# Kernel optimization log

Hardware: AMD Instinct MI355X
Metric: run time of the kernel (lower is better)

The kernel has to match this reference:

```python
import jax, jax.numpy as jnp
import numpy as np
import math

B, C, L = 64, 16, 4096
EMB, DEPTH, NEXP = 256, 2, 4
SHAPE, STRIDE = 8, 4
NPATCH = (L - SHAPE) // STRIDE + 1  # 1023
SPARSE = 0.5
NF = 32

def gelu(x):
    return jax.nn.gelu(x, approximate=False)

def conv1d(x, w, stride=1, pad=0):
    return jax.lax.conv_general_dilated(x, w, (stride,), [(pad, pad)],
                                        dimension_numbers=('NCH', 'OIH', 'NCH'))

def rmsnorm(x, g):
    # F.normalize(x, dim=-1) * gamma * sqrt(D)
    n = jnp.sqrt(jnp.sum(x * x, axis=-1, keepdims=True))
    return x / jnp.maximum(n, 1e-12) * g * (x.shape[-1] ** 0.5)

def setup_inputs():
    ks = jax.random.split(jax.random.key(0), 16)
    r = lambda i, s: jax.random.normal(ks[i], s, jnp.float32) * 0.02
    return dict(
        x=jax.random.normal(ks[0], (B, C, L), jnp.float32),
        epoch=100, warm_up=50,
        emb_w=r(1, (EMB, C, SHAPE)), emb_b=jnp.zeros((EMB,), jnp.float32),
        pos_embed=r(2, (1, NPATCH, EMB)),
        attn_w1=r(3, (EMB, 8)), attn_b1=jnp.zeros((8,), jnp.float32),
        attn_w2=r(4, (8, 1)), attn_b2=jnp.zeros((1,), jnp.float32),
        gate_w=r(5, (EMB, NEXP)), gate_b=jnp.zeros((NEXP,), jnp.float32),
        ex_w1=r(6, (NEXP, EMB, EMB)), ex_b1=jnp.zeros((NEXP, EMB), jnp.float32),
        ex_w2=r(7, (NEXP, EMB, EMB)), ex_b2=jnp.zeros((NEXP, EMB), jnp.float32),
        moe_gamma=jnp.ones((EMB,), jnp.float32),
        norm1_g=jnp.ones((DEPTH, EMB), jnp.float32),
        norm2_g=jnp.ones((DEPTH, EMB), jnp.float32),
        bott_w=r(8, (DEPTH, NF, EMB, 1)),
        conv_w39=r(9, (DEPTH, NF, NF, 39)),
        conv_w19=r(10, (DEPTH, NF, NF, 19)),
        conv_w9=r(11, (DEPTH, NF, NF, 9)),
        mp_w=r(12, (DEPTH, NF, EMB, 1)),
        bn_g=jnp.ones((DEPTH, 4 * NF), jnp.float32),
        bn_b=jnp.zeros((DEPTH, 4 * NF), jnp.float32),
        proj_w=r(13, (DEPTH, 4 * NF, EMB)),
        proj_b=jnp.zeros((DEPTH, EMB), jnp.float32),
        head_w=r(14, (EMB, 1)), head_b=jnp.zeros((1,), jnp.float32),
    )

def _forward(x, epoch, warm_up, emb_w, emb_b, pos_embed, attn_w1, attn_b1,
             attn_w2, attn_b2, gate_w, gate_b, ex_w1, ex_b1, ex_w2, ex_b2,
             moe_gamma, norm1_g, norm2_g, bott_w, conv_w39, conv_w19, conv_w9,
             mp_w, bn_g, bn_b, proj_w, proj_b, head_w, head_b):
    def attn(h):  # (B,N,D) -> (B,N,1) sigmoid importance scores
        return jax.nn.sigmoid(jnp.tanh(h @ attn_w1 + attn_b1) @ attn_w2 + attn_b2)

    def moe(h):  # top-1 routed MoE; compute all experts densely, select via one-hot
        Bm, Nm, D = h.shape
        hf = h.reshape(-1, D)  # (T, D)
        logits = jax.nn.softmax(hf @ gate_w + gate_b, axis=-1)  # (T, E)
        top_idx = jnp.argmax(logits, axis=-1)
        top_val = jnp.max(logits, axis=-1, keepdims=True)
        mid = gelu(jnp.einsum('td,edh->eth', hf, ex_w1) + ex_b1[:, None, :])
        ye = jnp.einsum('eth,ehd->etd', mid, ex_w2) + ex_b2[:, None, :]
        sel = jax.nn.one_hot(top_idx, NEXP, dtype=h.dtype)  # (T, E)
        out = jnp.einsum('etd,te->td', ye, sel)
        y = rmsnorm((hf + out * top_val).reshape(Bm, Nm, D), moe_gamma)
        imp = logits.sum(0)
        load = jnp.var(imp, ddof=1) / (imp.mean() ** 2 + 1e-10)
        return gelu(y), load

    def inception(xc, i):  # xc: (B, D, T) -> (B, 4*NF, T)
        xb = conv1d(xc, bott_w[i])  # bottleneck 1x1 -> NF channels
        mp = jax.lax.reduce_window(xc, -jnp.inf, jax.lax.max, (1, 1, 3),
                                   (1, 1, 1), [(0, 0), (0, 0), (1, 1)])
        out = jnp.concatenate([conv1d(xb, conv_w39[i], pad=19),
                               conv1d(xb, conv_w19[i], pad=9),
                               conv1d(xb, conv_w9[i], pad=4),
                               conv1d(mp, mp_w[i])], axis=1)
        # BatchNorm1d eval mode: running mean 0 / var 1, affine gamma/beta
        out = out * (bn_g[i] / np.float32(np.sqrt(1.0 + 1e-5)))[None, :, None] \
              + bn_b[i][None, :, None]
        return gelu(out)

    def incep_branch(h, i):  # (B,N,D) -> (B,N,D)
        io = inception(jnp.transpose(h, (0, 2, 1)), i)
        return jnp.transpose(io, (0, 2, 1)) @ proj_w[i] + proj_b[i]

    h = conv1d(x, emb_w, stride=STRIDE) + emb_b[None, :, None]  # (B, EMB, N)
    h = jnp.transpose(h, (0, 2, 1)) + pos_embed  # N == NPATCH -> no interp
    # pos_drop is identity at inference

    schedule = np.linspace(0.0, SPARSE, DEPTH)
    total_loss = jnp.zeros((), h.dtype)
    end_scores = None
    for i in range(DEPTH):
        ratio = 1.0 if epoch < warm_up else 1.0 - float(schedule[i])
        is_last = (i == DEPTH - 1)
        N = h.shape[1]
        x_n = rmsnorm(h, norm1_g[i])
        scores = attn(x_n)  # (B, N, 1)
        if ratio < 1.0 and N > 2:
            left_k = max(math.ceil(ratio * N), 1)
            xs = x_n * scores
            idx = jnp.sort(jax.lax.top_k(scores[..., 0], left_k)[1], axis=1)
            left_x = jnp.take_along_axis(xs, idx[:, :, None], axis=1)
            # sum of non-topk tokens == total sum minus topk sum
            extra = xs.sum(1, keepdims=True) - left_x.sum(1, keepdims=True)
            h = jnp.concatenate([left_x, extra], axis=1)  # (B, left_k+1, D)
            x_n2 = rmsnorm(h, norm2_g[i])
            moe_out, loss = moe(x_n2)
            h = h + moe_out + incep_branch(x_n2, i)
            total_loss = total_loss + loss
        else:
            h = x_n * scores
            h = h + incep_branch(rmsnorm(h, norm2_g[i]), i)
        if is_last:
            end_scores = attn(h)  # dropout identity; scores on pre-gelu x
        h = gelu(h)
    logits = h @ head_w + head_b  # (B, N', 1)
    cls = (logits * end_scores).mean(axis=1)  # (B, 1)
    return cls[..., 0], total_loss

def reference(x, epoch, warm_up, emb_w, emb_b, pos_embed, attn_w1, attn_b1,
              attn_w2, attn_b2, gate_w, gate_b, ex_w1, ex_b1, ex_w2, ex_b2,
              moe_gamma, norm1_g, norm2_g, bott_w, conv_w39, conv_w19, conv_w9,
              mp_w, bn_g, bn_b, proj_w, proj_b, head_w, head_b):
    return _forward(x, epoch, warm_up, emb_w, emb_b, pos_embed, attn_w1,
                    attn_b1, attn_w2, attn_b2, gate_w, gate_b, ex_w1, ex_b1,
                    ex_w2, ex_b2, moe_gamma, norm1_g, norm2_g, bott_w,
                    conv_w39, conv_w19, conv_w9, mp_w, bn_g, bn_b, proj_w,
                    proj_b, head_w, head_b)
```

## Files before the change

kernel.cpp:

```cpp
#include <hip/hip_runtime.h>
#include <math.h>

#define BB 64
#define EMB 256
#define N0 1023
#define N1 513
#define NTOK0 (BB * N0)
#define NTOK1 (BB * N1)
#define GCH 16

typedef __attribute__((ext_vector_type(8))) short short8;
typedef __attribute__((ext_vector_type(4))) float f32x4;

__device__ __forceinline__ float gelu_f(float x) {
    return 0.5f * x * (1.0f + erff(x * 0.7071067811865476f));
}

__device__ __forceinline__ float4 gelu4(float4 v) {
    return make_float4(gelu_f(v.x), gelu_f(v.y), gelu_f(v.z), gelu_f(v.w));
}

__device__ __forceinline__ float wave_reduce(float v) {
#pragma unroll
    for (int o = 32; o > 0; o >>= 1) v += __shfl_down(v, o, 64);
    return v;
}

__device__ __forceinline__ unsigned short f2bf(float f) {
    unsigned int u = __float_as_uint(f);
    u = (u + 0x7FFFu + ((u >> 16) & 1u)) >> 16;
    return (unsigned short)u;
}
__device__ __forceinline__ float bf2f(unsigned short h) {
    return __uint_as_float(((unsigned int)h) << 16);
}

__global__ void convert_bf16(const float* __restrict__ ew1, const float* __restrict__ ew2,
                             const float* __restrict__ pjw,
                             const float* __restrict__ cw39, const float* __restrict__ cw19,
                             const float* __restrict__ cw9, const float* __restrict__ embw,
                             const float* __restrict__ bott, const float* __restrict__ mpw,
                             unsigned short* __restrict__ w1t, unsigned short* __restrict__ w2t,
                             unsigned short* __restrict__ pjwb,
                             unsigned short* __restrict__ cwh, unsigned short* __restrict__ cwl,
                             unsigned short* __restrict__ ewh, unsigned short* __restrict__ ewl,
                             unsigned short* __restrict__ bth, unsigned short* __restrict__ btl,
                             unsigned short* __restrict__ mph, unsigned short* __restrict__ mpl,
                             float* __restrict__ imp, int* __restrict__ counts) {
    int idx = blockIdx.x * 256 + threadIdx.x;
    if (blockIdx.x == 0 && threadIdx.x >= 252) {
        int i = threadIdx.x - 252;
        imp[i] = 0.0f; counts[i] = 0;
    }
    if (idx < 262144) {
        int e = idx >> 16, r = idx & 65535, n = r >> 8, k = r & 255;
        w1t[idx] = f2bf(ew1[(e << 16) + (k << 8) + n]);
    } else if (idx < 524288) {
        int j = idx - 262144;
        int e = j >> 16, r = j & 65535, n = r >> 8, k = r & 255;
        w2t[j] = f2bf(ew2[(e << 16) + (k << 8) + n]);
    } else if (idx < 589824) {
        int j = idx - 524288;
        int d = j >> 15, r = j & 32767, n = r >> 7, k = r & 127;
        pjwb[j] = f2bf(pjw[(d << 15) + (k << 8) + n]);
    } else if (idx < 727040) {
        int j = idx - 589824;
        int d = j / 68608, r = j % 68608;
        const float* src; int KT, rr;
        if (r < 39936)      { src = cw39; KT = 39; rr = r; }
        else if (r < 59392) { src = cw19; KT = 19; rr = r - 39936; }
        else                { src = cw9;  KT = 9;  rr = r - 59392; }
        int KK = KT * 32;
        int fo = rr / KK, jj = rr % KK, k = jj >> 5, fi = jj & 31;
        float w = src[(((d * 32 + fo) * 32) + fi) * KT + k];
        unsigned short h = f2bf(w);
        cwh[j] = h;
        cwl[j] = f2bf(w - bf2f(h));
    } else if (idx < 759808) {
        int j = idx - 727040;
        float w = embw[j];
        unsigned short h = f2bf(w);
        ewh[j] = h;
        ewl[j] = f2bf(w - bf2f(h));
    } else if (idx < 776192) {
        int j = idx - 759808;
        float w = bott[j];
        unsigned short h = f2bf(w);
        bth[j] = h;
        btl[j] = f2bf(w - bf2f(h));
    } else if (idx < 792576) {
        int j = idx - 776192;
        float w = mpw[j];
        unsigned short h = f2bf(w);
        mph[j] = h;
        mpl[j] = f2bf(w - bf2f(h));
    }
}

__global__ __launch_bounds__(256, 2)
void embed_mfma(const float* __restrict__ x, const unsigned short* __restrict__ ewh,
                const unsigned short* __restrict__ ewl, const float* __restrict__ emb_b,
                const float* __restrict__ pos, float* __restrict__ A) {
    int b = blockIdx.y;
    int n0 = blockIdx.x * 64;
    __shared__ __align__(16) unsigned short tokh[64 * 128];
    __shared__ __align__(16) unsigned short tokl[64 * 128];
    int tid = threadIdx.x;
#pragma unroll
    for (int it = 0; it < 4; it++) {
        int idx = tid + it * 256;
        int m = idx & 63, c = idx >> 6;
        int tok = n0 + m;
        float v[8] = {0.f, 0.f, 0.f, 0.f, 0.f, 0.f, 0.f, 0.f};
        if (tok < N0) {
            const float* p = x + ((size_t)b * 16 + c) * 4096 + 4 * tok;
            float4 a = *(const float4*)p;
            float4 bq = *(const float4*)(p + 4);
            v[0] = a.x; v[1] = a.y; v[2] = a.z; v[3] = a.w;
            v[4] = bq.x; v[5] = bq.y; v[6] = bq.z; v[7] = bq.w;
        }
        short8 hv, lv;
#pragma unroll
        for (int j = 0; j < 8; j++) {
            unsigned short hh = f2bf(v[j]);
            hv[j] = (short)hh;
            lv[j] = (short)f2bf(v[j] - bf2f(hh));
        }
        int si = (m << 7) + ((c << 3) ^ ((m & 7) << 3));
        *(short8*)(&tokh[si]) = hv;
        *(short8*)(&tokl[si]) = lv;
    }
    __syncthreads();

    int lane = tid & 63, wid = tid >> 6;
    int nb = wid << 6;
    int arow = lane & 15;
    int kgrp = (lane >> 4) << 3;
    int rb = (lane >> 4) << 2;

    f32x4 acc[4][4];
#pragma unroll
    for (int mt = 0; mt < 4; mt++)
#pragma unroll
        for (int nt = 0; nt < 4; nt++) acc[mt][nt] = f32x4{0.f, 0.f, 0.f, 0.f};

    for (int ks = 0; ks < 4; ks++) {
        int kk = (ks << 5) + kgrp;
        short8 ah[4], al[4], bh[4], bl[4];
#pragma unroll
        for (int mt = 0; mt < 4; mt++) {
            int m = (mt << 4) + arow;
            int si = (m << 7) + (kk ^ ((m & 7) << 3));
            ah[mt] = *(const short8*)(&tokh[si]);
            al[mt] = *(const short8*)(&tokl[si]);
        }
#pragma unroll
        for (int nt = 0; nt < 4; nt++) {
            int n = nb + (nt << 4) + arow;
            bh[nt] = *(const short8*)(&ewh[(n << 7) + kk]);
            bl[nt] = *(const short8*)(&ewl[(n << 7) + kk]);
        }
#pragma unroll
        for (int mt = 0; mt < 4; mt++) {
#pragma unroll
            for (int nt = 0; nt < 4; nt++) {
                acc[mt][nt] = __builtin_amdgcn_mfma_f32_16x16x32_bf16(ah[mt], bh[nt], acc[mt][nt], 0, 0, 0);
                acc[mt][nt] = __builtin_amdgcn_mfma_f32_16x16x32_bf16(al[mt], bh[nt], acc[mt][nt], 0, 0, 0);
                acc[mt][nt] = __builtin_amdgcn_mfma_f32_16x16x32_bf16(ah[mt], bl[nt], acc[mt][nt], 0, 0, 0);
            }
        }
    }

    float eb[4];
#pragma unroll
    for (int nt = 0; nt < 4; nt++) eb[nt] = emb_b[nb + (nt << 4) + arow];
#pragma unroll
    for (int mt = 0; mt < 4; mt++) {
#pragma unroll
        for (int nt = 0; nt < 4; nt++) {
            int n = nb + (nt << 4) + arow;
#pragma unroll
            for (int r = 0; r < 4; r++) {
                int m = (mt << 4) + rb + r;
                int tok = n0 + m;
                if (tok < N0)
                    A[((size_t)b * N0 + tok) * 256 + n] =
                        acc[mt][nt][r] + eb[nt] + pos[(size_t)tok * 256 + n];
            }
        }
    }
}

__global__ void norm_attn_kernel(const float* __restrict__ in, float* __restrict__ outv,
                                 float* __restrict__ score_out, const float* __restrict__ g,
                                 const float* __restrict__ w1, const float* __restrict__ b1,
                                 const float* __restrict__ w2, const float* __restrict__ b2,
                                 int scale_out, int pregelu,
                                 float* __restrict__ outv2, const float* __restrict__ g2,
                                 int T) {
    int wid = threadIdx.x >> 6, lane = threadIdx.x & 63;
    int t = blockIdx.x * 4 + wid;
    if (t >= T) return;
    float4 v = ((const float4*)(in + (size_t)t * 256))[lane];
    if (pregelu) v = gelu4(v);
    float4 xn = v;
    if (g != nullptr) {
        float ss = v.x * v.x + v.y * v.y + v.z * v.z + v.w * v.w;
        ss = wave_reduce(ss);
        ss = __shfl(ss, 0, 64);
        float inv = 16.0f / fmaxf(sqrtf(ss), 1e-12f);
        float4 g4 = ((const float4*)g)[lane];
        xn.x = v.x * inv * g4.x; xn.y = v.y * inv * g4.y;
        xn.z = v.z * inv * g4.z; xn.w = v.w * inv * g4.w;
    }
    float p[8];
#pragma unroll
    for (int j = 0; j < 8; j++) p[j] = 0.0f;
    const float xv[4] = {xn.x, xn.y, xn.z, xn.w};
#pragma unroll
    for (int c = 0; c < 4; c++) {
        const float4* wr = (const float4*)(w1 + (4 * lane + c) * 8);
        float4 wa = wr[0], wb = wr[1];
        float xx = xv[c];
        p[0] += xx * wa.x; p[1] += xx * wa.y; p[2] += xx * wa.z; p[3] += xx * wa.w;
        p[4] += xx * wb.x; p[5] += xx * wb.y; p[6] += xx * wb.z; p[7] += xx * wb.w;
    }
#pragma unroll
    for (int j = 0; j < 8; j++) p[j] = wave_reduce(p[j]);
    float sc = 0.0f;
    if (lane == 0) {
        float z = b2[0];
#pragma unroll
        for (int j = 0; j < 8; j++) z += tanhf(p[j] + b1[j]) * w2[j];
        sc = 1.0f / (1.0f + expf(-z));
        if (score_out) score_out[t] = sc;
    }
    sc = __shfl(sc, 0, 64);
    if (outv) {
        float m = scale_out ? sc : 1.0f;
        float4 o = make_float4(xn.x * m, xn.y * m, xn.z * m, xn.w * m);
        ((float4*)(outv + (size_t)t * 256))[lane] = o;
    }
    if (outv2) {
        float ss2 = xn.x * xn.x + xn.y * xn.y + xn.z * xn.z + xn.w * xn.w;
        ss2 = wave_reduce(ss2);
        ss2 = __shfl(ss2, 0, 64);
        float inv2 = 16.0f / fmaxf(sqrtf(ss2), 1e-12f);
        float4 q4 = ((const float4*)g2)[lane];
        float4 o;
        o.x = xn.x * inv2 * q4.x; o.y = xn.y * inv2 * q4.y;
        o.z = xn.z * inv2 * q4.z; o.w = xn.w * inv2 * q4.w;
        ((float4*)(outv2 + (size_t)t * 256))[lane] = o;
    }
}

__global__ void rmsnorm_kernel(const float* __restrict__ in, float* __restrict__ out,
                               const float* __restrict__ g, int T) {
    int wid = threadIdx.x >> 6, lane = threadIdx.x & 63;
    int t = blockIdx.x * 4 + wid;
    if (t >= T) return;
    float4 v = ((const float4*)(in + (size_t)t * 256))[lane];
    float ss = v.x * v.x + v.y * v.y + v.z * v.z + v.w * v.w;
    ss = wave_reduce(ss);
    ss = __shfl(ss, 0, 64);
    float inv = 16.0f / fmaxf(sqrtf(ss), 1e-12f);
    float4 g4 = ((const float4*)g)[lane];
    float4 o;
    o.x = v.x * inv * g4.x; o.y = v.y * inv * g4.y;
    o.z = v.z * inv * g4.z; o.w = v.w * inv * g4.w;
    ((float4*)(out + (size_t)t * 256))[lane] = o;
}

__global__ __launch_bounds__(256, 2)
void pw_mfma(const float* __restrict__ xn, const unsigned short* __restrict__ bwh,
             const unsigned short* __restrict__ bwl, const unsigned short* __restrict__ mwh,
             const unsigned short* __restrict__ mwl, const float* __restrict__ bng,
             const float* __restrict__ bnb, float* __restrict__ xb,
             float* __restrict__ cat, int N) {
    int b = blockIdx.y;
    int t0 = blockIdx.x * 32;
    __shared__ __align__(16) unsigned short xth[34 * 256];
    __shared__ __align__(16) unsigned short xtl[34 * 256];
    __shared__ __align__(16) unsigned short xmh[32 * 256];
    __shared__ __align__(16) unsigned short xml[32 * 256];
    const float* xbase = xn + (size_t)b * N * 256;
    int tid = threadIdx.x;
    for (int idx = tid; idx < 34 * 32; idx += 256) {
        int r = idx >> 5, p = (idx & 31) << 3;
        int t = t0 - 1 + r;
        short8 hv, lv;
        if (t >= 0 && t < N) {
            const float4* q = (const float4*)(xbase + (size_t)t * 256 + p);
            float4 a = q[0], c = q[1];
            float v[8] = {a.x, a.y, a.z, a.w, c.x, c.y, c.z, c.w};
#pragma unroll
            for (int j = 0; j < 8; j++) {
                unsigned short hh = f2bf(v[j]);
                hv[j] = (short)hh;
                lv[j] = (short)f2bf(v[j] - bf2f(hh));
            }
        } else {
#pragma unroll
            for (int j = 0; j < 8; j++) { hv[j] = (short)0xFF80; lv[j] = 0; }
        }
        int si = (r << 8) + (p ^ ((r & 7) << 3));
        *(short8*)(&xth[si]) = hv;
        *(short8*)(&xtl[si]) = lv;
    }
    __syncthreads();
    for (int idx = tid; idx < 32 * 32; idx += 256) {
        int r = idx >> 5, p = (idx & 31) << 3;
        int s0 = ((r + 0) << 8) + (p ^ (((r + 0) & 7) << 3));
        int s1 = ((r + 1) << 8) + (p ^ (((r + 1) & 7) << 3));
        int s2 = ((r + 2) << 8) + (p ^ (((r + 2) & 7) << 3));
        short8 h0 = *(const short8*)(&xth[s0]), l0 = *(const short8*)(&xtl[s0]);
        short8 h1 = *(const short8*)(&xth[s1]), l1 = *(const short8*)(&xtl[s1]);
        short8 h2 = *(const short8*)(&xth[s2]), l2 = *(const short8*)(&xtl[s2]);
        short8 hv, lv;
#pragma unroll
        for (int j = 0; j < 8; j++) {
            float a = bf2f((unsigned short)h0[j]) + bf2f((unsigned short)l0[j]);
            float c = bf2f((unsigned short)h1[j]) + bf2f((unsigned short)l1[j]);
            float d = bf2f((unsigned short)h2[j]) + bf2f((unsigned short)l2[j]);
            float m = fmaxf(fmaxf(a, c), d);
            unsigned short hh = f2bf(m);
            hv[j] = (short)hh;
            lv[j] = (short)f2bf(m - bf2f(hh));
        }
        int si = (r << 8) + (p ^ ((r & 7) << 3));
        *(short8*)(&xmh[si]) = hv;
        *(short8*)(&xml[si]) = lv;
    }
    __syncthreads();

    int lane = tid & 63, wid = tid >> 6;
    int mt = wid & 1, path = wid >> 1;
    int arow = lane & 15, kgrp = (lane >> 4) << 3, rb = (lane >> 4) << 2;
    const unsigned short* Wh = path ? mwh : bwh;
    const unsigned short* Wl = path ? mwl : bwl;
    f32x4 acc[2];
    acc[0] = f32x4{0.f, 0.f, 0.f, 0.f};
    acc[1] = f32x4{0.f, 0.f, 0.f, 0.f};

    int m = (mt << 4) + arow;
    int rowA = path ? m : (m + 1);
    const unsigned short* Ah = path ? xmh : xth;
    const unsigned short* Al = path ? xml : xtl;
    for (int ks = 0; ks < 8; ks++) {
        int kk = (ks << 5) + kgrp;
        int si = (rowA << 8) + (kk ^ ((rowA & 7) << 3));
        short8 ah = *(const short8*)(&Ah[si]);
        short8 al = *(const short8*)(&Al[si]);
#pragma unroll
        for (int nt = 0; nt < 2; nt++) {
            int n = (nt << 4) + arow;
            short8 bh = *(const short8*)(&Wh[n * 256 + kk]);
            short8 bl = *(const short8*)(&Wl[n * 256 + kk]);
            acc[nt] = __builtin_amdgcn_mfma_f32_16x16x32_bf16(ah, bh, acc[nt], 0, 0, 0);
            acc[nt] = __builtin_amdgcn_mfma_f32_16x16x32_bf16(al, bh, acc[nt], 0, 0, 0);
            acc[nt] = __builtin_amdgcn_mfma_f32_16x16x32_bf16(ah, bl, acc[nt], 0, 0, 0);
        }
    }

    const float BN_DIV = 1.0000050f;
    if (path == 0) {
#pragma unroll
        for (int nt = 0; nt < 2; nt++) {
            int n = (nt << 4) + arow;
#pragma unroll
            for (int r = 0; r < 4; r++) {
                int t = t0 + (mt << 4) + rb + r;
                if (t < N) xb[((size_t)b * N + t) * 32 + n] = acc[nt][r];
            }
        }
    } else {
#pragma unroll
        for (int nt = 0; nt < 2; nt++) {
            int n = (nt << 4) + arow;
            float scl = bng[96 + n] / BN_DIV;
            float sh = bnb[96 + n];
#pragma unroll
            for (int r = 0; r < 4; r++) {
                int t = t0 + (mt << 4) + rb + r;
                if (t < N)
                    cat[((size_t)b * N + t) * 128 + 96 + n] = gelu_f(acc[nt][r] * scl + sh);
            }
        }
    }
}

__global__ __launch_bounds__(256, 4)
void conv_mfma(const float* __restrict__ xb, const unsigned short* __restrict__ wh,
               const unsigned short* __restrict__ wl, const float* __restrict__ bng,
               const float* __restrict__ bnb, float* __restrict__ cat, int N) {
    int b = blockIdx.y;
    int t0 = blockIdx.x * 64;
    __shared__ __align__(16) unsigned short tokh[104 * 40];
    __shared__ __align__(16) unsigned short tokl[104 * 40];
    const float* xbase = xb + (size_t)b * N * 32;
    int tid = threadIdx.x;
    for (int idx = tid; idx < 104 * 16; idx += 256) {
        int r = idx >> 4, p = (idx & 15) << 1;
        int t = t0 - 19 + r;
        float vx = 0.f, vy = 0.f;
        if (t >= 0 && t < N) {
            const float2 v = *(const float2*)(xbase + (size_t)t * 32 + p);
            vx = v.x; vy = v.y;
        }
        unsigned short h0 = f2bf(vx), h1 = f2bf(vy);
        unsigned short l0 = f2bf(vx - bf2f(h0)), l1 = f2bf(vy - bf2f(h1));
        *(unsigned int*)(&tokh[r * 40 + p]) = (unsigned)h0 | ((unsigned)h1 << 16);
        *(unsigned int*)(&tokl[r * 40 + p]) = (unsigned)l0 | ((unsigned)l1 << 16);
    }
    __syncthreads();
    int lane = tid & 63, wid = tid >> 6;
    int arow = lane & 15, kgrp = (lane >> 4) << 3;
    int rb = (lane >> 4) << 2;
    f32x4 acc[3][2];
#pragma unroll
    for (int i = 0; i < 3; i++) {
        acc[i][0] = f32x4{0.f, 0.f, 0.f, 0.f};
        acc[i][1] = f32x4{0.f, 0.f, 0.f, 0.f};
    }

#define CONV_BR(KT, BOFF, WOFF, BR)                                                        \
    {                                                                                      \
        const int KK = (KT) * 32;                                                          \
        int r0 = (WOFF) + wid * 16 + arow;                                                 \
        const unsigned short* whp = wh + (BOFF) + arow * KK + kgrp;                        \
        const unsigned short* wlp = wl + (BOFF) + arow * KK + kgrp;                        \
        for (int k = 0; k < (KT); k++) {                                                   \
            short8 ah = *(const short8*)(&tokh[(r0 + k) * 40 + kgrp]);                     \
            short8 al = *(const short8*)(&tokl[(r0 + k) * 40 + kgrp]);                     \
            short8 bh0 = *(const short8*)(&whp[k * 32]);                                   \
            short8 bl0 = *(const short8*)(&wlp[k * 32]);                                   \
            short8 bh1 = *(const short8*)(&whp[16 * KK + k * 32]);                         \
            short8 bl1 = *(const short8*)(&wlp[16 * KK + k * 32]);                         \
            acc[BR][0] = __builtin_amdgcn_mfma_f32_16x16x32_bf16(ah, bh0, acc[BR][0], 0, 0, 0); \
            acc[BR][1] = __builtin_amdgcn_mfma_f32_16x16x32_bf16(ah, bh1, acc[BR][1], 0, 0, 0); \
            acc[BR][0] = __builtin_amdgcn_mfma_f32_16x16x32_bf16(al, bh0, acc[BR][0], 0, 0, 0); \
            acc[BR][1] = __builtin_amdgcn_mfma_f32_16x16x32_bf16(al, bh1, acc[BR][1], 0, 0, 0); \
            acc[BR][0] = __builtin_amdgcn_mfma_f32_16x16x32_bf16(ah, bl0, acc[BR][0], 0, 0, 0); \
            acc[BR][1] = __builtin_amdgcn_mfma_f32_16x16x32_bf16(ah, bl1, acc[BR][1], 0, 0, 0); \
        }                                                                                  \
    }

    CONV_BR(39, 0, 0, 0)
    CONV_BR(19, 39936, 10, 1)
    CONV_BR(9, 59392, 15, 2)
#undef CONV_BR

    const float BN_DIV = 1.0000050f;
    const int COFFS[3] = {0, 32, 64};
#pragma unroll
    for (int br = 0; br < 3; br++) {
#pragma unroll
        for (int nt = 0; nt < 2; nt++) {
            int fo = COFFS[br] + nt * 16 + arow;
            float scl = bng[fo] / BN_DIV;
            float sh = bnb[fo];
#pragma unroll
            for (int r = 0; r < 4; r++) {
                int t = t0 + wid * 16 + rb + r;
                if (t < N)
                    cat[((size_t)b * N + t) * 128 + fo] = gelu_f(acc[br][nt][r] * scl + sh);
            }
        }
    }
}

__global__ __launch_bounds__(256, 2)
void proj_mfma(const float* __restrict__ cat, const unsigned short* __restrict__ pjt,
               const float* __restrict__ pb, float* __restrict__ A, int TN) {
    int t0 = blockIdx.x * 64;
    __shared__ __align__(16) unsigned short tokh[64 * 128];
    __shared__ __align__(16) unsigned short tokl[64 * 128];
    int tid = threadIdx.x;
#pragma unroll
    for (int it = 0; it < 4; it++) {
        int idx = tid + it * 256;
        int m = idx >> 4, c = idx & 15;
        int t = t0 + m;
        float v[8] = {0.f, 0.f, 0.f, 0.f, 0.f, 0.f, 0.f, 0.f};
        if (t < TN) {
            const float4* q = (const float4*)(cat + (size_t)t * 128 + (c << 3));
            float4 a = q[0], bq = q[1];
            v[0] = a.x; v[1] = a.y; v[2] = a.z; v[3] = a.w;
            v[4] = bq.x; v[5] = bq.y; v[6] = bq.z; v[7] = bq.w;
        }
        short8 hv, lv;
#pragma unroll
        for (int j = 0; j < 8; j++) {
            unsigned short hh = f2bf(v[j]);
            hv[j] = (short)hh;
            lv[j] = (short)f2bf(v[j] - bf2f(hh));
        }
        int si = (m << 7) + ((c << 3) ^ ((m & 7) << 3));
        *(short8*)(&tokh[si]) = hv;
        *(short8*)(&tokl[si]) = lv;
    }
    __syncthreads();

    int lane = tid & 63, wid = tid >> 6;
    int nb = wid << 6;
    int arow = lane & 15;
    int kgrp = (lane >> 4) << 3;
    int rb = (lane >> 4) << 2;

    f32x4 acc[4][4];
#pragma unroll
    for (int mt = 0; mt < 4; mt++)
#pragma unroll
        for (int nt = 0; nt < 4; nt++) acc[mt][nt] = f32x4{0.f, 0.f, 0.f, 0.f};

    for (int ks = 0; ks < 4; ks++) {
        int kk = (ks << 5) + kgrp;
        short8 ah[4], al[4], bw[4];
#pragma unroll
        for (int mt = 0; mt < 4; mt++) {
            int m = (mt << 4) + arow;
            int si = (m << 7) + (kk ^ ((m & 7) << 3));
            ah[mt] = *(const short8*)(&tokh[si]);
            al[mt] = *(const short8*)(&tokl[si]);
        }
#pragma unroll
        for (int nt = 0; nt < 4; nt++) {
            int n = nb + (nt << 4) + arow;
            bw[nt] = *(const short8*)(&pjt[(n << 7) + kk]);
        }
#pragma unroll
        for (int mt = 0; mt < 4; mt++) {
#pragma unroll
            for (int nt = 0; nt < 4; nt++) {
                acc[mt][nt] = __builtin_amdgcn_mfma_f32_16x16x32_bf16(ah[mt], bw[nt], acc[mt][nt], 0, 0, 0);
                acc[mt][nt] = __builtin_amdgcn_mfma_f32_16x16x32_bf16(al[mt], bw[nt], acc[mt][nt], 0, 0, 0);
            }
        }
    }

    float bias[4];
#pragma unroll
    for (int nt = 0; nt < 4; nt++) bias[nt] = pb[nb + (nt << 4) + arow];
#pragma unroll
    for (int mt = 0; mt < 4; mt++) {
#pragma unroll
        for (int nt = 0; nt < 4; nt++) {
            int n = nb + (nt << 4) + arow;
#pragma unroll
            for (int r = 0; r < 4; r++) {
                int t = t0 + (mt << 4) + rb + r;
                if (t < TN) {
                    float* ap = A + (size_t)t * 256 + n;
                    *ap += acc[mt][nt][r] + bias[nt];
                }
            }
        }
    }
}

__global__ __launch_bounds__(1024) void topk_kernel(const float* __restrict__ s,
                                                    int* __restrict__ selpos) {
    int b = blockIdx.x;
    int tid = threadIdx.x;
    __shared__ float srt[1024];
    __shared__ int buf[1024];
    __shared__ int Gtot_s;
    float val = (tid < N0) ? s[(size_t)b * N0 + tid] : -INFINITY;
    srt[tid] = val;
    __syncthreads();
    for (int ksz = 2; ksz <= 1024; ksz <<= 1) {
        for (int j = ksz >> 1; j > 0; j >>= 1) {
            int ixj = tid ^ j;
            if (ixj > tid) {
                float a = srt[tid], c = srt[ixj];
                bool up = ((tid & ksz) == 0);
                if ((a > c) == up) { srt[tid] = c; srt[ixj] = a; }
            }
            __syncthreads();
        }
    }
    float thr = srt[512];
    __syncthreads();
    int isG = (val > thr) ? 1 : 0;
    int isE = (val == thr) ? 1 : 0;
    buf[tid] = isG;
    __syncthreads();
    for (int off = 1; off < 1024; off <<= 1) {
        int cur = buf[tid];
        int add = (tid >= off) ? buf[tid - off] : 0;
        __syncthreads();
        buf[tid] = cur + add;
        __syncthreads();
    }
    if (tid == 0) Gtot_s = buf[1023];
    __syncthreads();
    int Gtot = Gtot_s;
    int Eneed = 512 - Gtot;
    buf[tid] = isE;
    __syncthreads();
    for (int off = 1; off < 1024; off <<= 1) {
        int cur = buf[tid];
        int add = (tid >= off) ? buf[tid - off] : 0;
        __syncthreads();
        buf[tid] = cur + add;
        __syncthreads();
    }
    int eqExcl = buf[tid] - isE;
    int sel = (isG || (isE && eqExcl < Eneed)) ? 1 : 0;
    __syncthreads();
    buf[tid] = sel;
    __syncthreads();
    for (int off = 1; off < 1024; off <<= 1) {
        int cur = buf[tid];
        int add = (tid >= off) ? buf[tid - off] : 0;
        __syncthreads();
        buf[tid] = cur + add;
        __syncthreads();
    }
    int pos = buf[tid] - sel;
    selpos[b * 1024 + tid] = sel ? pos : -1;
}

__global__ void scatter_kernel(const float* __restrict__ xn, const float* __restrict__ s,
                               const int* __restrict__ selpos, float* __restrict__ A,
                               float* __restrict__ part) {
    int b = blockIdx.y;
    int chunk = blockIdx.x;
    int wid = threadIdx.x >> 6, lane = threadIdx.x & 63;
    int t0 = chunk * 64;
    __shared__ float sl[64];
    __shared__ int pl[64];
    if (threadIdx.x < 64) {
        int t = t0 + threadIdx.x;
        sl[threadIdx.x] = (t < N0) ? s[(size_t)b * N0 + t] : 0.0f;
        pl[threadIdx.x] = (t < N0) ? selpos[b * 1024 + t] : -1;
    }
    __syncthreads();
    const float* xbase = xn + ((size_t)b * N0 + t0) * 256;
    float* obase = A + (size_t)b * N1 * 256;
    float4 nonsel = make_float4(0.f, 0.f, 0.f, 0.f);
    int tmax = (t0 + 64 <= N0) ? 64 : (N0 - t0);
    for (int i = wid; i < tmax; i += 4) {
        float sc = sl[i];
        float4 v = ((const float4*)(xbase + (size_t)i * 256))[lane];
        v.x *= sc; v.y *= sc; v.z *= sc; v.w *= sc;
        int p = pl[i];
        if (p >= 0) ((float4*)(obase + (size_t)p * 256))[lane] = v;
        else { nonsel.x += v.x; nonsel.y += v.y; nonsel.z += v.z; nonsel.w += v.w; }
    }
    ((float4*)(part + ((size_t)(b * GCH + chunk) * 4 + wid) * 256))[lane] = nonsel;
}

__global__ void extra_kernel(const float* __restrict__ part, float* __restrict__ A) {
    int b = blockIdx.x, d = threadIdx.x;
    float acc = 0.0f;
    for (int c = 0; c < GCH * 4; c++) acc += part[((size_t)b * GCH * 4 + c) * 256 + d];
    A[((size_t)b * N1 + 512) * 256 + d] = acc;
}

__global__ void gate_kernel(const float* __restrict__ xn2, const float* __restrict__ gw,
                            const float* __restrict__ gb, float* __restrict__ topval,
                            int* __restrict__ buckets, int* __restrict__ counts,
                            float* __restrict__ imp, int T) {
    int tid = threadIdx.x;
    int t = blockIdx.x * 256 + tid;
    __shared__ float4 gws[256];
    __shared__ int lcount[4];
    __shared__ int lbase[4];
    __shared__ float limp[4];
    gws[tid] = ((const float4*)gw)[tid];
    if (tid < 4) { lcount[tid] = 0; limp[tid] = 0.0f; }
    __syncthreads();
    bool valid = (t < T);
    float a0 = 0, a1 = 0, a2 = 0, a3 = 0;
    if (valid) {
        const float4* xb4 = (const float4*)(xn2 + (size_t)t * 256);
#pragma unroll 8
        for (int d4 = 0; d4 < 64; d4++) {
            float4 xv = xb4[d4];
            float4 w0 = gws[4 * d4], w1 = gws[4 * d4 + 1];
            float4 w2 = gws[4 * d4 + 2], w3 = gws[4 * d4 + 3];
            a0 += xv.x * w0.x + xv.y * w1.x + xv.z * w2.x + xv.w * w3.x;
            a1 += xv.x * w0.y + xv.y * w1.y + xv.z * w2.y + xv.w * w3.y;
            a2 += xv.x * w0.z + xv.y * w1.z + xv.z * w2.z + xv.w * w3.z;
            a3 += xv.x * w0.w + xv.y * w1.w + xv.z * w2.w + xv.w * w3.w;
        }
    }
    float q0 = 0, q1 = 0, q2 = 0, q3 = 0;
    int eid = 0;
    int lrank = 0;
    if (valid) {
        float l0 = a0 + gb[0], l1 = a1 + gb[1], l2 = a2 + gb[2], l3 = a3 + gb[3];
        float m = fmaxf(fmaxf(l0, l1), fmaxf(l2, l3));
        float e0 = expf(l0 - m), e1 = expf(l1 - m), e2 = expf(l2 - m), e3 = expf(l3 - m);
        float ssum = e0 + e1 + e2 + e3;
        q0 = e0 / ssum; q1 = e1 / ssum; q2 = e2 / ssum; q3 = e3 / ssum;
        float bv = q0;
        if (q1 > bv) { bv = q1; eid = 1; }
        if (q2 > bv) { bv = q2; eid = 2; }
        if (q3 > bv) { bv = q3; eid = 3; }
        topval[t] = bv;
        lrank = atomicAdd(&lcount[eid], 1);
    }
    float r0 = wave_reduce(q0), r1 = wave_reduce(q1);
    float r2 = wave_reduce(q2), r3 = wave_reduce(q3);
    if ((tid & 63) == 0) {
        atomicAdd(&limp[0], r0); atomicAdd(&limp[1], r1);
        atomicAdd(&limp[2], r2); atomicAdd(&limp[3], r3);
    }
    __syncthreads();
    if (tid < 4) {
        lbase[tid] = atomicAdd(&counts[tid], lcount[tid]);
        atomicAdd(&imp[tid], limp[tid]);
    }
    __syncthreads();
    if (valid) buckets[eid * T + lbase[eid] + lrank] = t;
}

#define FFN_KLOOP(WPTR)                                                                    \
    for (int ks = 0; ks < 8; ks++) {                                                       \
        int kk = (ks << 5) + kgrp;                                                         \
        short8 ah[4], al[4], bw[4];                                                        \
        _Pragma("unroll")                                                                  \
        for (int mt = 0; mt < 4; mt++) {                                                   \
            int m = (mt << 4) + arow;                                                      \
            int si = (m << 8) + (kk ^ ((m & 7) << 3));                                     \
            ah[mt] = *(const short8*)(&tokh[si]);                                          \
            al[mt] = *(const short8*)(&tokl[si]);                                          \
        }                                                                                  \
        _Pragma("unroll")                                                                  \
        for (int nt = 0; nt < 4; nt++)                                                     \
            bw[nt] = *(const short8*)(&WPTR[((size_t)(nb + (nt << 4) + arow) << 8) + kk]); \
        _Pragma("unroll")                                                                  \
        for (int mt = 0; mt < 4; mt++) {                                                   \
            _Pragma("unroll")                                                              \
            for (int nt = 0; nt < 4; nt++) {                                               \
                acc[mt][nt] = __builtin_amdgcn_mfma_f32_16x16x32_bf16(                     \
                    ah[mt], bw[nt], acc[mt][nt], 0, 0, 0);                                 \
                acc[mt][nt] = __builtin_amdgcn_mfma_f32_16x16x32_bf16(                     \
                    al[mt], bw[nt], acc[mt][nt], 0, 0, 0);                                 \
            }                                                                              \
        }                                                                                  \
    }

__global__ __launch_bounds__(256, 2)
void ffn_kernel(const float* __restrict__ xn2, const unsigned short* __restrict__ w1t,
                const float* __restrict__ b1, const unsigned short* __restrict__ w2t,
                const float* __restrict__ b2, const float* __restrict__ topval,
                const int* __restrict__ buckets, const int* __restrict__ counts,
                float* __restrict__ C, int T) {
    int e = blockIdx.y;
    int cnt = counts[e];
    int base = blockIdx.x * 64;
    if (base >= cnt) return;
    __shared__ __align__(16) unsigned short tokh[64 * 256];
    __shared__ __align__(16) unsigned short tokl[64 * 256];
    __shared__ int tids[64];
    __shared__ float tv[64];
    int tid = threadIdx.x;
    if (tid < 64) {
        int idx = base + tid;
        int t = (idx < cnt) ? buckets[e * T + idx] : -1;
        tids[tid] = t;
        tv[tid] = (t >= 0) ? topval[t] : 0.0f;
    }
    __syncthreads();
#pragma unroll
    for (int it = 0; it < 8; it++) {
        int cc = tid + it * 256;
        int m = cc >> 5, d0 = (cc & 31) << 3;
        int t = tids[m];
        float4 a = make_float4(0.f, 0.f, 0.f, 0.f), b = a;
        if (t >= 0) {
            const float4* p = (const float4*)(xn2 + (size_t)t * 256 + d0);
            a = p[0]; b = p[1];
        }
        float v[8] = {a.x, a.y, a.z, a.w, b.x, b.y, b.z, b.w};
        short8 hv, lv;
#pragma unroll
        for (int j = 0; j < 8; j++) {
            unsigned short hh = f2bf(v[j]);
            hv[j] = (short)hh;
            lv[j] = (short)f2bf(v[j] - bf2f(hh));
        }
        int si = (m << 8) + (d0 ^ ((m & 7) << 3));
        *(short8*)(&tokh[si]) = hv;
        *(short8*)(&tokl[si]) = lv;
    }
    __syncthreads();

    int lane = tid & 63, wid = tid >> 6;
    int nb = wid << 6;
    int arow = lane & 15;
    int kgrp = (lane >> 4) << 3;
    int rb = (lane >> 4) << 2;
    const unsigned short* W1 = w1t + ((size_t)e << 16);
    const unsigned short* W2 = w2t + ((size_t)e << 16);

    f32x4 acc[4][4];
#pragma unroll
    for (int mt = 0; mt < 4; mt++)
#pragma unroll
        for (int nt = 0; nt < 4; nt++) acc[mt][nt] = f32x4{0.f, 0.f, 0.f, 0.f};

    FFN_KLOOP(W1)

    float b1v[4];
#pragma unroll
    for (int nt = 0; nt < 4; nt++) b1v[nt] = b1[(e << 8) + nb + (nt << 4) + arow];
    __syncthreads();
#pragma unroll
    for (int mt = 0; mt < 4; mt++) {
#pragma unroll
        for (int nt = 0; nt < 4; nt++) {
            int kd = nb + (nt << 4) + arow;
#pragma unroll
            for (int r = 0; r < 4; r++) {
                int m = (mt << 4) + rb + r;
                float mid = gelu_f(acc[mt][nt][r] + b1v[nt]);
                unsigned short hh = f2bf(mid);
                int si = (m << 8) + (kd ^ ((m & 7) << 3));
                tokh[si] = hh;
                tokl[si] = f2bf(mid - bf2f(hh));
            }
        }
    }
    __syncthreads();

#pragma unroll
    for (int mt = 0; mt < 4; mt++)
#pragma unroll
        for (int nt = 0; nt < 4; nt++) acc[mt][nt] = f32x4{0.f, 0.f, 0.f, 0.f};

    FFN_KLOOP(W2)

    float b2v[4];
#pragma unroll
    for (int nt = 0; nt < 4; nt++) b2v[nt] = b2[(e << 8) + nb + (nt << 4) + arow];
#pragma unroll
    for (int mt = 0; mt < 4; mt++) {
        int tt[4]; float tvv[4];
#pragma unroll
        for (int r = 0; r < 4; r++) {
            int m = (mt << 4) + rb + r;
            tt[r] = tids[m];
            tvv[r] = tv[m];
        }
#pragma unroll
        for (int nt = 0; nt < 4; nt++) {
            int n = nb + (nt << 4) + arow;
#pragma unroll
            for (int r = 0; r < 4; r++) {
                int t = tt[r];
                if (t >= 0) {
                    float val = acc[mt][nt][r] + b2v[nt];
                    C[(size_t)t * 256 + n] =
                        xn2[(size_t)t * 256 + n] + val * tvv[r];
                }
            }
        }
    }
}

__global__ void moe_add_kernel(const float* __restrict__ C, float* __restrict__ A,
                               const float* __restrict__ gamma, int T) {
    int wid = threadIdx.x >> 6, lane = threadIdx.x & 63;
    int t = blockIdx.x * 4 + wid;
    if (t >= T) return;
    float4 v = ((const float4*)(C + (size_t)t * 256))[lane];
    float ss = v.x * v.x + v.y * v.y + v.z * v.z + v.w * v.w;
    ss = wave_reduce(ss);
    ss = __shfl(ss, 0, 64);
    float inv = 16.0f / fmaxf(sqrtf(ss), 1e-12f);
    float4 g4 = ((const float4*)gamma)[lane];
    float4* ap = (float4*)(A + (size_t)t * 256) + lane;
    float4 a = *ap;
    a.x += gelu_f(v.x * inv * g4.x); a.y += gelu_f(v.y * inv * g4.y);
    a.z += gelu_f(v.z * inv * g4.z); a.w += gelu_f(v.w * inv * g4.w);
    *ap = a;
}

__global__ void endhead_kernel(const float* __restrict__ A, const float* __restrict__ w1,
                               const float* __restrict__ b1, const float* __restrict__ w2,
                               const float* __restrict__ b2, const float* __restrict__ hw,
                               const float* __restrict__ hb, float* __restrict__ contrib,
                               int T) {
    int wid = threadIdx.x >> 6, lane = threadIdx.x & 63;
    int t = blockIdx.x * 4 + wid;
    if (t >= T) return;
    float4 v = ((const float4*)(A + (size_t)t * 256))[lane];
    float p[8];
#pragma unroll
    for (int j = 0; j < 8; j++) p[j] = 0.0f;
    const float xv[4] = {v.x, v.y, v.z, v.w};
#pragma unroll
    for (int c = 0; c < 4; c++) {
        const float4* wr = (const float4*)(w1 + (4 * lane + c) * 8);
        float4 wa = wr[0], wb = wr[1];
        float xx = xv[c];
        p[0] += xx * wa.x; p[1] += xx * wa.y; p[2] += xx * wa.z; p[3] += xx * wa.w;
        p[4] += xx * wb.x; p[5] += xx * wb.y; p[6] += xx * wb.z; p[7] += xx * wb.w;
    }
    float4 h4 = ((const float4*)hw)[lane];
    float hp = gelu_f(v.x) * h4.x + gelu_f(v.y) * h4.y + gelu_f(v.z) * h4.z + gelu_f(v.w) * h4.w;
#pragma unroll
    for (int j = 0; j < 8; j++) p[j] = wave_reduce(p[j]);
    hp = wave_reduce(hp);
    if (lane == 0) {
        float z = b2[0];
#pragma unroll
        for (int j = 0; j < 8; j++) z += tanhf(p[j] + b1[j]) * w2[j];
        float sc = 1.0f / (1.0f + expf(-z));
        contrib[t] = (hp + hb[0]) * sc * (1.0f / (float)N1);
    }
}

__global__ void finalsum_kernel(const float* __restrict__ contrib,
                                const float* __restrict__ imp, float* __restrict__ out) {
    int b = blockIdx.x, tid = threadIdx.x;
    __shared__ float red[4];
    const float* cb = contrib + (size_t)b * N1;
    float v = cb[tid] + cb[256 + tid];
    if (tid == 0) v += cb[512];
    float s = wave_reduce(v);
    int wid = tid >> 6, lane = tid & 63;
    if (lane == 0) red[wid] = s;
    __syncthreads();
    if (tid == 0) {
        out[b] = red[0] + red[1] + red[2] + red[3];
        if (b == 0) {
            float i0 = imp[0], i1 = imp[1], i2 = imp[2], i3 = imp[3];
            float mean = (i0 + i1 + i2 + i3) * 0.25f;
            float var = ((i0 - mean) * (i0 - mean) + (i1 - mean) * (i1 - mean) +
                         (i2 - mean) * (i2 - mean) + (i3 - mean) * (i3 - mean)) / 3.0f;
            out[64] = var / (mean * mean + 1e-10f);
        }
    }
}

extern "C" void kernel_launch(void* const* d_in, const int* in_sizes, int n_in,
                              void* d_out, int out_size, void* d_ws, size_t ws_size,
                              hipStream_t stream) {
    const float* x    = (const float*)d_in[0];
    const float* embw = (const float*)d_in[3];
    const float* embb = (const float*)d_in[4];
    const float* pos  = (const float*)d_in[5];
    const float* aw1  = (const float*)d_in[6];
    const float* ab1  = (const float*)d_in[7];
    const float* aw2  = (const float*)d_in[8];
    const float* ab2  = (const float*)d_in[9];
    const float* gw   = (const float*)d_in[10];
    const float* gb   = (const float*)d_in[11];
    const float* ew1  = (const float*)d_in[12];
    const float* eb1  = (const float*)d_in[13];
    const float* ew2  = (const float*)d_in[14];
    const float* eb2  = (const float*)d_in[15];
    const float* mg   = (const float*)d_in[16];
    const float* n1g  = (const float*)d_in[17];
    const float* n2g  = (const float*)d_in[18];
    const float* bott = (const float*)d_in[19];
    const float* cw39 = (const float*)d_in[20];
    const float* cw19 = (const float*)d_in[21];
    const float* cw9  = (const float*)d_in[22];
    const float* mpw  = (const float*)d_in[23];
    const float* bng  = (const float*)d_in[24];
    const float* bnb  = (const float*)d_in[25];
    const float* pjw  = (const float*)d_in[26];
    const float* pjb  = (const float*)d_in[27];
    const float* hw   = (const float*)d_in[28];
    const float* hb   = (const float*)d_in[29];
    float* out = (float*)d_out;

    float* W = (float*)d_ws;
    size_t off = 0;
    auto alloc = [&](size_t n) { float* p = W + off; off += n; return p; };
    float* A    = alloc((size_t)NTOK0 * 256);
    float* Bb   = alloc((size_t)NTOK0 * 256);
    float* CD   = alloc((size_t)NTOK1 * 256);
    float* XB   = alloc((size_t)NTOK0 * 32);
    float* sS   = alloc(NTOK0);
    float* ctb  = alloc(NTOK1);
    float* tval = alloc(NTOK1);
    float* imp  = alloc(4);
    float* part = alloc((size_t)BB * GCH * 4 * 256);
    off = (off + 3) & ~(size_t)3;
    unsigned short* w1t  = (unsigned short*)(W + off); off += 262144 / 2;
    unsigned short* w2t  = (unsigned short*)(W + off); off += 262144 / 2;
    unsigned short* pjwb = (unsigned short*)(W + off); off += 65536 / 2;
    unsigned short* cwh  = (unsigned short*)(W + off); off += 137216 / 2;
    unsigned short* cwl  = (unsigned short*)(W + off); off += 137216 / 2;
    unsigned short* ewh  = (unsigned short*)(W + off); off += 32768 / 2;
    unsigned short* ewl  = (unsigned short*)(W + off); off += 32768 / 2;
    unsigned short* bth  = (unsigned short*)(W + off); off += 16384 / 2;
    unsigned short* btl  = (unsigned short*)(W + off); off += 16384 / 2;
    unsigned short* mph  = (unsigned short*)(W + off); off += 16384 / 2;
    unsigned short* mpl  = (unsigned short*)(W + off); off += 16384 / 2;
    int* selpos  = (int*)(W + off); off += (size_t)BB * 1024;
    int* buckets = (int*)(W + off); off += (size_t)4 * NTOK1;
    int* counts  = (int*)(W + off); off += 4;

    convert_bf16<<<3096, 256, 0, stream>>>(ew1, ew2, pjw, cw39, cw19, cw9, embw, bott, mpw,
                                           w1t, w2t, pjwb, cwh, cwl, ewh, ewl,
                                           bth, btl, mph, mpl, imp, counts);

    embed_mfma<<<dim3(16, BB), 256, 0, stream>>>(x, ewh, ewl, embb, pos, A);
    norm_attn_kernel<<<NTOK0 / 4, 256, 0, stream>>>(A, A, nullptr, n1g, aw1, ab1, aw2, ab2,
                                                    1, 0, Bb, n2g, NTOK0);
    pw_mfma<<<dim3(32, BB), 256, 0, stream>>>(Bb, bth, btl, mph, mpl, bng, bnb, XB, CD, N0);
    conv_mfma<<<dim3(16, BB), 256, 0, stream>>>(XB, cwh, cwl, bng, bnb, CD, N0);
    proj_mfma<<<NTOK0 / 64, 256, 0, stream>>>(CD, pjwb, pjb, A, NTOK0);

    norm_attn_kernel<<<NTOK0 / 4, 256, 0, stream>>>(A, Bb, sS, n1g + 256, aw1, ab1, aw2, ab2,
                                                    0, 1, nullptr, nullptr, NTOK0);
    topk_kernel<<<BB, 1024, 0, stream>>>(sS, selpos);
    scatter_kernel<<<dim3(GCH, BB), 256, 0, stream>>>(Bb, sS, selpos, A, part);
    extra_kernel<<<BB, 256, 0, stream>>>(part, A);
    rmsnorm_kernel<<<NTOK1 / 4, 256, 0, stream>>>(A, Bb, n2g + 256, NTOK1);
    gate_kernel<<<(NTOK1 + 255) / 256, 256, 0, stream>>>(Bb, gw, gb, tval, buckets, counts, imp,
                                                         NTOK1);
    ffn_kernel<<<dim3((NTOK1 + 63) / 64, 4), 256, 0, stream>>>(Bb, w1t, eb1, w2t, eb2, tval,
                                                               buckets, counts, CD, NTOK1);
    moe_add_kernel<<<NTOK1 / 4, 256, 0, stream>>>(CD, A, mg, NTOK1);
    pw_mfma<<<dim3((N1 + 31) / 32, BB), 256, 0, stream>>>(Bb, bth + 8192, btl + 8192,
                                                          mph + 8192, mpl + 8192,
                                                          bng + 128, bnb + 128, XB, CD, N1);
    conv_mfma<<<dim3(9, BB), 256, 0, stream>>>(XB, cwh + 68608, cwl + 68608,
                                               bng + 128, bnb + 128, CD, N1);
    proj_mfma<<<NTOK1 / 64, 256, 0, stream>>>(CD, pjwb + 32768, pjb + 256, A, NTOK1);
    endhead_kernel<<<NTOK1 / 4, 256, 0, stream>>>(A, aw1, ab1, aw2, ab2, hw, hb, ctb, NTOK1);
    finalsum_kernel<<<BB, 256, 0, stream>>>(ctb, imp, out);
}
```

Before: 801.1 us.

## Double conv tile to 128 tokens per block and swizzle LDS layout

The conv_mfma kernel now covers 128 tokens per block instead of 64, and each wave computes two 16-row M tiles. Every B-fragment weight load from global memory is therefore reused across twice as many MFMAs. The LDS token buffer drops its 40-element padded stride for a 32-element stride with an XOR swizzle, meant to avoid bank conflicts on the A-fragment reads. In exchange, the kernel holds twice as many accumulators, occupancy is lowered to 2 blocks per CU, and the grid is halved, which may leave too few blocks to keep all CUs busy.

```diff
diff --git a/kernel.cpp b/kernel.cpp
--- a/kernel.cpp
+++ b/kernel.cpp
@@ -389,59 +389,72 @@
     }
 }
 
-__global__ __launch_bounds__(256, 4)
+__global__ __launch_bounds__(256, 2)
 void conv_mfma(const float* __restrict__ xb, const unsigned short* __restrict__ wh,
                const unsigned short* __restrict__ wl, const float* __restrict__ bng,
                const float* __restrict__ bnb, float* __restrict__ cat, int N) {
     int b = blockIdx.y;
-    int t0 = blockIdx.x * 64;
-    __shared__ __align__(16) unsigned short tokh[104 * 40];
-    __shared__ __align__(16) unsigned short tokl[104 * 40];
+    int t0 = blockIdx.x * 128;
+    __shared__ __align__(16) unsigned short tokh[167 * 32];
+    __shared__ __align__(16) unsigned short tokl[167 * 32];
     const float* xbase = xb + (size_t)b * N * 32;
     int tid = threadIdx.x;
-    for (int idx = tid; idx < 104 * 16; idx += 256) {
-        int r = idx >> 4, p = (idx & 15) << 1;
+    for (int idx = tid; idx < 167 * 16; idx += 256) {
+        int r = idx >> 4, c = (idx & 15) << 1;
         int t = t0 - 19 + r;
         float vx = 0.f, vy = 0.f;
         if (t >= 0 && t < N) {
-            const float2 v = *(const float2*)(xbase + (size_t)t * 32 + p);
+            const float2 v = *(const float2*)(xbase + (size_t)t * 32 + c);
             vx = v.x; vy = v.y;
         }
         unsigned short h0 = f2bf(vx), h1 = f2bf(vy);
         unsigned short l0 = f2bf(vx - bf2f(h0)), l1 = f2bf(vy - bf2f(h1));
-        *(unsigned int*)(&tokh[r * 40 + p]) = (unsigned)h0 | ((unsigned)h1 << 16);
-        *(unsigned int*)(&tokl[r * 40 + p]) = (unsigned)l0 | ((unsigned)l1 << 16);
+        int si = (r << 5) + ((((c >> 3) ^ ((r >> 1) & 3)) << 3) | (c & 7));
+        *(unsigned int*)(&tokh[si]) = (unsigned)h0 | ((unsigned)h1 << 16);
+        *(unsigned int*)(&tokl[si]) = (unsigned)l0 | ((unsigned)l1 << 16);
     }
     __syncthreads();
     int lane = tid & 63, wid = tid >> 6;
-    int arow = lane & 15, kgrp = (lane >> 4) << 3;
-    int rb = (lane >> 4) << 2;
-    f32x4 acc[3][2];
-#pragma unroll
-    for (int i = 0; i < 3; i++) {
-        acc[i][0] = f32x4{0.f, 0.f, 0.f, 0.f};
-        acc[i][1] = f32x4{0.f, 0.f, 0.f, 0.f};
-    }
-
+    int arow = lane & 15, g = lane >> 4, kgrp = g << 3;
+    int rb = g << 2;
+    f32x4 acc[3][2][2];
+#pragma unroll
+    for (int i = 0; i < 3; i++)
+#pragma unroll
+        for (int m = 0; m < 2; m++) {
+            acc[i][m][0] = f32x4{0.f, 0.f, 0.f, 0.f};
+            acc[i][m][1] = f32x4{0.f, 0.f, 0.f, 0.f};
+        }
+
+#define SIA(row) (((row) << 5) + ((g ^ (((row) >> 1) & 3)) << 3))
 #define CONV_BR(KT, BOFF, WOFF, BR)                                                        \
     {                                                                                      \
         const int KK = (KT) * 32;                                                          \
-        int r0 = (WOFF) + wid * 16 + arow;                                                 \
+        int r0 = (WOFF) + wid * 32 + arow;                                                 \
         const unsigned short* whp = wh + (BOFF) + arow * KK + kgrp;                        \
         const unsigned short* wlp = wl + (BOFF) + arow * KK + kgrp;                        \
         for (int k = 0; k < (KT); k++) {                                                   \
-            short8 ah = *(const short8*)(&tokh[(r0 + k) * 40 + kgrp]);                     \
-            short8 al = *(const short8*)(&tokl[(r0 + k) * 40 + kgrp]);                     \
+            int ra = r0 + k, rc = r0 + 16 + k;                                             \
+            short8 ah0 = *(const short8*)(&tokh[SIA(ra)]);                                 \
+            short8 al0 = *(const short8*)(&tokl[SIA(ra)]);                                 \
+            short8 ah1 = *(const short8*)(&tokh[SIA(rc)]);                                 \
+            short8 al1 = *(const short8*)(&tokl[SIA(rc)]);                                 \
             short8 bh0 = *(const short8*)(&whp[k * 32]);                                   \
             short8 bl0 = *(const short8*)(&wlp[k * 32]);                                   \
             short8 bh1 = *(const short8*)(&whp[16 * KK + k * 32]);                         \
             short8 bl1 = *(const short8*)(&wlp[16 * KK + k * 32]);                         \
-            acc[BR][0] = __builtin_amdgcn_mfma_f32_16x16x32_bf16(ah, bh0, acc[BR][0], 0, 0, 0); \
-            acc[BR][1] = __builtin_amdgcn_mfma_f32_16x16x32_bf16(ah, bh1, acc[BR][1], 0, 0, 0); \
-            acc[BR][0] = __builtin_amdgcn_mfma_f32_16x16x32_bf16(al, bh0, acc[BR][0], 0, 0, 0); \
-            acc[BR][1] = __builtin_amdgcn_mfma_f32_16x16x32_bf16(al, bh1, acc[BR][1], 0, 0, 0); \
-            acc[BR][0] = __builtin_amdgcn_mfma_f32_16x16x32_bf16(ah, bl0, acc[BR][0], 0, 0, 0); \
-            acc[BR][1] = __builtin_amdgcn_mfma_f32_16x16x32_bf16(ah, bl1, acc[BR][1], 0, 0, 0); \
+            acc[BR][0][0] = __builtin_amdgcn_mfma_f32_16x16x32_bf16(ah0, bh0, acc[BR][0][0], 0, 0, 0); \
+            acc[BR][0][1] = __builtin_amdgcn_mfma_f32_16x16x32_bf16(ah0, bh1, acc[BR][0][1], 0, 0, 0); \
+            acc[BR][0][0] = __builtin_amdgcn_mfma_f32_16x16x32_bf16(al0, bh0, acc[BR][0][0], 0, 0, 0); \
+            acc[BR][0][1] = __builtin_amdgcn_mfma_f32_16x16x32_bf16(al0, bh1, acc[BR][0][1], 0, 0, 0); \
+            acc[BR][0][0] = __builtin_amdgcn_mfma_f32_16x16x32_bf16(ah0, bl0, acc[BR][0][0], 0, 0, 0); \
+            acc[BR][0][1] = __builtin_amdgcn_mfma_f32_16x16x32_bf16(ah0, bl1, acc[BR][0][1], 0, 0, 0); \
+            acc[BR][1][0] = __builtin_amdgcn_mfma_f32_16x16x32_bf16(ah1, bh0, acc[BR][1][0], 0, 0, 0); \
+            acc[BR][1][1] = __builtin_amdgcn_mfma_f32_16x16x32_bf16(ah1, bh1, acc[BR][1][1], 0, 0, 0); \
+            acc[BR][1][0] = __builtin_amdgcn_mfma_f32_16x16x32_bf16(al1, bh0, acc[BR][1][0], 0, 0, 0); \
+            acc[BR][1][1] = __builtin_amdgcn_mfma_f32_16x16x32_bf16(al1, bh1, acc[BR][1][1], 0, 0, 0); \
+            acc[BR][1][0] = __builtin_amdgcn_mfma_f32_16x16x32_bf16(ah1, bl0, acc[BR][1][0], 0, 0, 0); \
+            acc[BR][1][1] = __builtin_amdgcn_mfma_f32_16x16x32_bf16(ah1, bl1, acc[BR][1][1], 0, 0, 0); \
         }                                                                                  \
     }
 
@@ -449,21 +462,26 @@
     CONV_BR(19, 39936, 10, 1)
     CONV_BR(9, 59392, 15, 2)
 #undef CONV_BR
+#undef SIA
 
     const float BN_DIV = 1.0000050f;
     const int COFFS[3] = {0, 32, 64};
 #pragma unroll
     for (int br = 0; br < 3; br++) {
 #pragma unroll
-        for (int nt = 0; nt < 2; nt++) {
-            int fo = COFFS[br] + nt * 16 + arow;
-            float scl = bng[fo] / BN_DIV;
-            float sh = bnb[fo];
-#pragma unroll
-            for (int r = 0; r < 4; r++) {
-                int t = t0 + wid * 16 + rb + r;
-                if (t < N)
-                    cat[((size_t)b * N + t) * 128 + fo] = gelu_f(acc[br][nt][r] * scl + sh);
+        for (int mt = 0; mt < 2; mt++) {
+#pragma unroll
+            for (int nt = 0; nt < 2; nt++) {
+                int fo = COFFS[br] + nt * 16 + arow;
+                float scl = bng[fo] / BN_DIV;
+                float sh = bnb[fo];
+#pragma unroll
+                for (int r = 0; r < 4; r++) {
+                    int t = t0 + wid * 32 + mt * 16 + rb + r;
+                    if (t < N)
+                        cat[((size_t)b * N + t) * 128 + fo] =
+                            gelu_f(acc[br][mt][nt][r] * scl + sh);
+                }
             }
         }
     }
@@ -1007,7 +1025,7 @@
     norm_attn_kernel<<<NTOK0 / 4, 256, 0, stream>>>(A, A, nullptr, n1g, aw1, ab1, aw2, ab2,
                                                     1, 0, Bb, n2g, NTOK0);
     pw_mfma<<<dim3(32, BB), 256, 0, stream>>>(Bb, bth, btl, mph, mpl, bng, bnb, XB, CD, N0);
-    conv_mfma<<<dim3(16, BB), 256, 0, stream>>>(XB, cwh, cwl, bng, bnb, CD, N0);
+    conv_mfma<<<dim3(8, BB), 256, 0, stream>>>(XB, cwh, cwl, bng, bnb, CD, N0);
     proj_mfma<<<NTOK0 / 64, 256, 0, stream>>>(CD, pjwb, pjb, A, NTOK0);
 
     norm_attn_kernel<<<NTOK0 / 4, 256, 0, stream>>>(A, Bb, sS, n1g + 256, aw1, ab1, aw2, ab2,
@@ -1024,8 +1042,8 @@
     pw_mfma<<<dim3((N1 + 31) / 32, BB), 256, 0, stream>>>(Bb, bth + 8192, btl + 8192,
                                                           mph + 8192, mpl + 8192,
                                                           bng + 128, bnb + 128, XB, CD, N1);
-    conv_mfma<<<dim3(9, BB), 256, 0, stream>>>(XB, cwh + 68608, cwl + 68608,
-                                               bng + 128, bnb + 128, CD, N1);
+    conv_mfma<<<dim3((N1 + 127) / 128, BB), 256, 0, stream>>>(XB, cwh + 68608, cwl + 68608,
+                                                              bng + 128, bnb + 128, CD, N1);
     proj_mfma<<<NTOK1 / 64, 256, 0, stream>>>(CD, pjwb + 32768, pjb + 256, A, NTOK1);
     endhead_kernel<<<NTOK1 / 4, 256, 0, stream>>>(A, aw1, ab1, aw2, ab2, hw, hb, ctb, NTOK1);
     finalsum_kernel<<<BB, 256, 0, stream>>>(ctb, imp, out);
```

After: 889.9 us. 11.1% more time.
